# Kernel optimization log

Hardware: AMD Instinct MI355X
Metric: run time of the kernel (lower is better)

The kernel has to match this reference:

```python
import jax, jax.numpy as jnp
import numpy as np


def setup_inputs() -> dict:
    key = jax.random.key(0)
    k1, k2, k3 = jax.random.split(key, 3)
    B, C, H, W = 64, 512, 28, 28
    K = 32
    std = 1.0 / (K * C) ** 0.5
    x = jax.random.normal(k1, (B, C, H, W), dtype=jnp.float32)
    codewords = jax.random.uniform(k2, (K, C), dtype=jnp.float32, minval=-std, maxval=std)
    scale = jax.random.uniform(k3, (K,), dtype=jnp.float32, minval=-1.0, maxval=0.0)
    return {"x": x, "codewords": codewords, "scale": scale}


def reference(x, codewords, scale):
    # x: (B, C, H, W) -> descriptors (B, N, C)
    B, C, H, W = x.shape
    K = codewords.shape[0]
    xd = x.reshape(B, C, H * W).transpose(0, 2, 1)  # (B, N, C)

    # scaled L2: scale_k * ||x_n - c_k||^2, expanded without (B,N,K,C) intermediate
    x_sq = jnp.sum(xd * xd, axis=-1, keepdims=True)            # (B, N, 1)
    c_sq = jnp.sum(codewords * codewords, axis=-1)             # (K,)
    xc = jnp.einsum("bnc,kc->bnk", xd, codewords)              # (B, N, K)
    dist = scale * (x_sq - 2.0 * xc + c_sq)                    # (B, N, K)

    A = jax.nn.softmax(dist, axis=2)                           # (B, N, K)

    # encoded_k = sum_n A[b,n,k] * (x[b,n] - c[k])
    wx = jnp.einsum("bnk,bnc->bkc", A, xd)                     # (B, K, C)
    wsum = jnp.sum(A, axis=1)                                  # (B, K)
    encoded = wx - wsum[:, :, None] * codewords[None, :, :]    # (B, K, C)
    return encoded
```

## Files before the change

kernel.cpp:

```cpp
#include <hip/hip_runtime.h>
#include <hip/hip_bf16.h>

#define BB 64
#define CC 512
#define NPIX 784
#define KK 32
#define NSPL 7
#define PXB 112
#define CW_S 520
#define XA_S 136

typedef __attribute__((ext_vector_type(8))) short short8;
typedef __attribute__((ext_vector_type(4))) float floatx4;
typedef __attribute__((ext_vector_type(4))) unsigned short ushort4v;

#define OFF_WP 0
#define OFF_WS (NSPL*BB*KK*CC)

__device__ __forceinline__ unsigned short f2bf(float f) {
    union { float f; unsigned u; } v; v.f = f;
    return (unsigned short)((v.u + 0x7FFFu + ((v.u >> 16) & 1u)) >> 16);
}
__device__ __forceinline__ float bf2f(unsigned short h) {
    union { unsigned u; float f; } v; v.u = ((unsigned)h) << 16; return v.f;
}

__global__ __launch_bounds__(256) void k_fused(const float* __restrict__ x,
                                               const float* __restrict__ cw,
                                               const float* __restrict__ scale,
                                               float* __restrict__ ws)
{
    __shared__ __align__(16) unsigned char u8[128 * XA_S * 2];
    __shared__ __align__(16) unsigned short A_l[KK * XA_S];
    __shared__ float csq_p[8][KK];
    __shared__ float csq_l[KK];
    __shared__ float wred[KK][8];

    unsigned short* cs = (unsigned short*)u8;
    unsigned short* xs = (unsigned short*)u8;

    const int t     = threadIdx.x;
    const int lane  = t & 63;
    const int w     = t >> 6;
    const int col   = lane & 15;
    const int quad  = lane >> 4;
    const int split = blockIdx.x;
    const int b     = blockIdx.y;
    const int p0    = split * PXB;

#pragma unroll 4
    for (int j = 0; j < 16; ++j) {
        const int qidx = t + j * 256;
        const int row = qidx >> 7, qc = qidx & 127;
        const float4 v = *(const float4*)&cw[row * CC + qc * 4];
        ushort4v p; p.x = f2bf(v.x); p.y = f2bf(v.y); p.z = f2bf(v.z); p.w = f2bf(v.w);
        *(ushort4v*)&cs[row * CW_S + qc * 4] = p;
    }
    __syncthreads();
    {
        const int k = t & 31, part = t >> 5;
        float s = 0.f;
        for (int i = 0; i < 64; ++i) {
            const float v = bf2f(cs[k * CW_S + part * 64 + i]);
            s += v * v;
        }
        csq_p[part][k] = s;
    }
    __syncthreads();
    if (t < KK) {
        float s = 0.f;
#pragma unroll
        for (int p = 0; p < 8; ++p) s += csq_p[p][t];
        csq_l[t] = s;
    }
    __syncthreads();

    const float s0 = scale[col], s1 = scale[col + 16];
    const float q0 = csq_l[col], q1 = csq_l[col + 16];

    for (int pt = w; pt < NSPL; pt += 4) {
        const int px = p0 + pt * 16 + col;
        const float* xb = x + (size_t)b * CC * NPIX + px;

        floatx4 acc0 = {0.f, 0.f, 0.f, 0.f};
        floatx4 acc1 = {0.f, 0.f, 0.f, 0.f};
        float xsqp = 0.f;
        float va[8], vb[8];

#pragma unroll
        for (int j = 0; j < 8; ++j) va[j] = xb[(size_t)(quad * 8 + j) * NPIX];

#pragma unroll
        for (int kc = 0; kc < 16; kc += 2) {
            {
                const int cb = (kc + 1) * 32 + quad * 8;
#pragma unroll
                for (int j = 0; j < 8; ++j) vb[j] = xb[(size_t)(cb + j) * NPIX];
            }
            {
#pragma unroll
                for (int j = 0; j < 8; ++j) xsqp += va[j] * va[j];
                short8 a;
#pragma unroll
                for (int j = 0; j < 8; ++j) a[j] = (short)f2bf(va[j]);
                const int cb0 = kc * 32 + quad * 8;
                const short8 b0 = *(const short8*)&cs[col * CW_S + cb0];
                const short8 b1 = *(const short8*)&cs[(col + 16) * CW_S + cb0];
                acc0 = __builtin_amdgcn_mfma_f32_16x16x32_bf16(a, b0, acc0, 0, 0, 0);
                acc1 = __builtin_amdgcn_mfma_f32_16x16x32_bf16(a, b1, acc1, 0, 0, 0);
            }
            if (kc + 2 < 16) {
                const int cb = (kc + 2) * 32 + quad * 8;
#pragma unroll
                for (int j = 0; j < 8; ++j) va[j] = xb[(size_t)(cb + j) * NPIX];
            }
            {
#pragma unroll
                for (int j = 0; j < 8; ++j) xsqp += vb[j] * vb[j];
                short8 a;
#pragma unroll
                for (int j = 0; j < 8; ++j) a[j] = (short)f2bf(vb[j]);
                const int cb1 = (kc + 1) * 32 + quad * 8;
                const short8 b0 = *(const short8*)&cs[col * CW_S + cb1];
                const short8 b1 = *(const short8*)&cs[(col + 16) * CW_S + cb1];
                acc0 = __builtin_amdgcn_mfma_f32_16x16x32_bf16(a, b0, acc0, 0, 0, 0);
                acc1 = __builtin_amdgcn_mfma_f32_16x16x32_bf16(a, b1, acc1, 0, 0, 0);
            }
        }

        xsqp += __shfl_xor(xsqp, 16);
        xsqp += __shfl_xor(xsqp, 32);

#pragma unroll
        for (int r = 0; r < 4; ++r) {
            const float xq = __shfl(xsqp, quad * 4 + r);
            const float d0 = s0 * (xq + q0 - 2.f * acc0[r]);
            const float d1 = s1 * (xq + q1 - 2.f * acc1[r]);
            float mx = fmaxf(d0, d1);
            mx = fmaxf(mx, __shfl_xor(mx, 1));
            mx = fmaxf(mx, __shfl_xor(mx, 2));
            mx = fmaxf(mx, __shfl_xor(mx, 4));
            mx = fmaxf(mx, __shfl_xor(mx, 8));
            const float e0 = __expf(d0 - mx), e1 = __expf(d1 - mx);
            float sm = e0 + e1;
            sm += __shfl_xor(sm, 1);
            sm += __shfl_xor(sm, 2);
            sm += __shfl_xor(sm, 4);
            sm += __shfl_xor(sm, 8);
            const float inv = 1.f / sm;
            const int pxl = pt * 16 + quad * 4 + r;
            A_l[col * XA_S + pxl]        = f2bf(e0 * inv);
            A_l[(col + 16) * XA_S + pxl] = f2bf(e1 * inv);
        }
    }
    __syncthreads();

    {
        const int k = t >> 3, part = t & 7;
        float s = 0.f;
#pragma unroll 7
        for (int i = 0; i < 14; ++i) s += bf2f(A_l[k * XA_S + part * 14 + i]);
        wred[k][part] = s;
    }
    {
        const ushort4v z = {0, 0, 0, 0};
        if (t < 128) *(ushort4v*)&A_l[(t >> 2) * XA_S + PXB + (t & 3) * 4] = z;
#pragma unroll
        for (int jj = 0; jj < 2; ++jj) {
            const int q = t + jj * 256;
            *(ushort4v*)&xs[(q >> 2) * XA_S + PXB + (q & 3) * 4] = z;
        }
    }
    __syncthreads();

    if (t < KK) {
        float s = 0.f;
#pragma unroll
        for (int p = 0; p < 8; ++p) s += wred[t][p];
        ws[OFF_WS + (size_t)(split * BB + b) * KK + t] = s;
    }

    const float* xbase = x + (size_t)b * CC * NPIX + p0;
    float* Wp = ws + OFF_WP;

    for (int cch = 0; cch < 4; ++cch) {
#pragma unroll 2
        for (int j = 0; j < 14; ++j) {
            const int q = t + j * 256;
            const int row = q / 28, pq = q - row * 28;
            const float4 v = *(const float4*)&xbase[(size_t)(cch * 128 + row) * NPIX + pq * 4];
            ushort4v p; p.x = f2bf(v.x); p.y = f2bf(v.y); p.z = f2bf(v.z); p.w = f2bf(v.w);
            *(ushort4v*)&xs[row * XA_S + pq * 4] = p;
        }
        __syncthreads();

        floatx4 a00 = {0.f,0.f,0.f,0.f}, a01 = {0.f,0.f,0.f,0.f};
        floatx4 a10 = {0.f,0.f,0.f,0.f}, a11 = {0.f,0.f,0.f,0.f};
#pragma unroll
        for (int ks = 0; ks < 4; ++ks) {
            const int off = ks * 32 + quad * 8;
            const short8 av0 = *(const short8*)&A_l[col * XA_S + off];
            const short8 av1 = *(const short8*)&A_l[(col + 16) * XA_S + off];
            const short8 bv0 = *(const short8*)&xs[(w * 32 + col) * XA_S + off];
            const short8 bv1 = *(const short8*)&xs[(w * 32 + 16 + col) * XA_S + off];
            a00 = __builtin_amdgcn_mfma_f32_16x16x32_bf16(av0, bv0, a00, 0, 0, 0);
            a10 = __builtin_amdgcn_mfma_f32_16x16x32_bf16(av1, bv0, a10, 0, 0, 0);
            a01 = __builtin_amdgcn_mfma_f32_16x16x32_bf16(av0, bv1, a01, 0, 0, 0);
            a11 = __builtin_amdgcn_mfma_f32_16x16x32_bf16(av1, bv1, a11, 0, 0, 0);
        }

        const size_t sb = (size_t)(split * BB + b) * KK;
        const int cb = cch * 128 + w * 32;
#pragma unroll
        for (int r = 0; r < 4; ++r) {
            const int k0 = quad * 4 + r;
            Wp[(sb + k0) * CC + cb + col]           = a00[r];
            Wp[(sb + k0) * CC + cb + 16 + col]      = a01[r];
            Wp[(sb + k0 + 16) * CC + cb + col]      = a10[r];
            Wp[(sb + k0 + 16) * CC + cb + 16 + col] = a11[r];
        }
        __syncthreads();
    }
}

__global__ __launch_bounds__(256) void k3(const float* __restrict__ cw,
                                          const float* __restrict__ ws,
                                          float* __restrict__ out)
{
    const int idx = blockIdx.x * 256 + threadIdx.x;
    const int c4 = idx & 127;
    const int k  = (idx >> 7) & 31;
    const int b  = idx >> 12;

    const float* Wp = ws + OFF_WP;
    float4 s = make_float4(0.f, 0.f, 0.f, 0.f);
#pragma unroll
    for (int sp = 0; sp < NSPL; ++sp) {
        const float4 v = *(const float4*)&Wp[((size_t)(sp * BB + b) * KK + k) * CC + c4 * 4];
        s.x += v.x; s.y += v.y; s.z += v.z; s.w += v.w;
    }
    float wsum = 0.f;
#pragma unroll
    for (int sp = 0; sp < NSPL; ++sp) wsum += ws[OFF_WS + (size_t)(sp * BB + b) * KK + k];

    const float4 c4f = *(const float4*)&cw[k * CC + c4 * 4];
    float4 o;
    o.x = s.x - wsum * c4f.x;
    o.y = s.y - wsum * c4f.y;
    o.z = s.z - wsum * c4f.z;
    o.w = s.w - wsum * c4f.w;
    *(float4*)&out[(size_t)idx * 4] = o;
}

extern "C" void kernel_launch(void* const* d_in, const int* in_sizes, int n_in,
                              void* d_out, int out_size, void* d_ws, size_t ws_size,
                              hipStream_t stream) {
    const float* x     = (const float*)d_in[0];
    const float* cw    = (const float*)d_in[1];
    const float* scale = (const float*)d_in[2];
    float* out = (float*)d_out;
    float* ws  = (float*)d_ws;

    k_fused<<<dim3(NSPL, BB), dim3(256), 0, stream>>>(x, cw, scale, ws);
    k3<<<dim3(BB * KK * CC / 4 / 256), dim3(256), 0, stream>>>(cw, ws, out);
}
```

Baseline: 185.4 us.

## Split pixels into 13 blocks of 64 with one pixel tile per wave

Each block now covers 64 pixels instead of 112, giving 13 splits per batch instead of 7. Each of the four waves handles exactly one 16-pixel tile, and the tail past 784 pixels is handled by clamped loads and zero-masked writes. This replaces the separate padding pass and moves a barrier. The aim is more blocks for better GPU occupancy and less per-block serial work. In exchange it writes more partial results to the workspace (13 splits instead of 7), which the reduction kernel must read back. The codebook bf16 conversion and norm work is also repeated in more blocks.

```diff
diff --git a/kernel.cpp b/kernel.cpp
--- a/kernel.cpp
+++ b/kernel.cpp
@@ -5,10 +5,10 @@
 #define CC 512
 #define NPIX 784
 #define KK 32
-#define NSPL 7
-#define PXB 112
+#define NSPL 13
+#define PXB 64
 #define CW_S 520
-#define XA_S 136
+#define XS2_S 72
 
 typedef __attribute__((ext_vector_type(8))) short short8;
 typedef __attribute__((ext_vector_type(4))) float floatx4;
@@ -30,8 +30,8 @@
                                                const float* __restrict__ scale,
                                                float* __restrict__ ws)
 {
-    __shared__ __align__(16) unsigned char u8[128 * XA_S * 2];
-    __shared__ __align__(16) unsigned short A_l[KK * XA_S];
+    __shared__ __align__(16) unsigned char u8[KK * CW_S * 2];
+    __shared__ __align__(16) unsigned short A_l[KK * XS2_S];
     __shared__ float csq_p[8][KK];
     __shared__ float csq_l[KK];
     __shared__ float wred[KK][8];
@@ -78,8 +78,9 @@
     const float s0 = scale[col], s1 = scale[col + 16];
     const float q0 = csq_l[col], q1 = csq_l[col + 16];
 
-    for (int pt = w; pt < NSPL; pt += 4) {
-        const int px = p0 + pt * 16 + col;
+    {
+        const int pxg = p0 + w * 16 + col;
+        const int px = (pxg < NPIX) ? pxg : (NPIX - 1);
         const float* xb = x + (size_t)b * CC * NPIX + px;
 
         floatx4 acc0 = {0.f, 0.f, 0.f, 0.f};
@@ -133,6 +134,7 @@
 
 #pragma unroll
         for (int r = 0; r < 4; ++r) {
+            const int pl = w * 16 + quad * 4 + r;
             const float xq = __shfl(xsqp, quad * 4 + r);
             const float d0 = s0 * (xq + q0 - 2.f * acc0[r]);
             const float d1 = s1 * (xq + q1 - 2.f * acc1[r]);
@@ -148,9 +150,9 @@
             sm += __shfl_xor(sm, 4);
             sm += __shfl_xor(sm, 8);
             const float inv = 1.f / sm;
-            const int pxl = pt * 16 + quad * 4 + r;
-            A_l[col * XA_S + pxl]        = f2bf(e0 * inv);
-            A_l[(col + 16) * XA_S + pxl] = f2bf(e1 * inv);
+            const bool valid = (p0 + pl) < NPIX;
+            A_l[col * XS2_S + pl]        = valid ? f2bf(e0 * inv) : (unsigned short)0;
+            A_l[(col + 16) * XS2_S + pl] = valid ? f2bf(e1 * inv) : (unsigned short)0;
         }
     }
     __syncthreads();
@@ -158,21 +160,11 @@
     {
         const int k = t >> 3, part = t & 7;
         float s = 0.f;
-#pragma unroll 7
-        for (int i = 0; i < 14; ++i) s += bf2f(A_l[k * XA_S + part * 14 + i]);
+#pragma unroll
+        for (int i = 0; i < 8; ++i) s += bf2f(A_l[k * XS2_S + part * 8 + i]);
         wred[k][part] = s;
     }
-    {
-        const ushort4v z = {0, 0, 0, 0};
-        if (t < 128) *(ushort4v*)&A_l[(t >> 2) * XA_S + PXB + (t & 3) * 4] = z;
-#pragma unroll
-        for (int jj = 0; jj < 2; ++jj) {
-            const int q = t + jj * 256;
-            *(ushort4v*)&xs[(q >> 2) * XA_S + PXB + (q & 3) * 4] = z;
-        }
-    }
-    __syncthreads();
-
+    __syncthreads();
     if (t < KK) {
         float s = 0.f;
 #pragma unroll
@@ -184,25 +176,29 @@
     float* Wp = ws + OFF_WP;
 
     for (int cch = 0; cch < 4; ++cch) {
+        __syncthreads();
 #pragma unroll 2
-        for (int j = 0; j < 14; ++j) {
+        for (int j = 0; j < 8; ++j) {
             const int q = t + j * 256;
-            const int row = q / 28, pq = q - row * 28;
-            const float4 v = *(const float4*)&xbase[(size_t)(cch * 128 + row) * NPIX + pq * 4];
-            ushort4v p; p.x = f2bf(v.x); p.y = f2bf(v.y); p.z = f2bf(v.z); p.w = f2bf(v.w);
-            *(ushort4v*)&xs[row * XA_S + pq * 4] = p;
+            const int row = q >> 4, pq = q & 15;
+            ushort4v p;
+            if (p0 + pq * 4 < NPIX) {
+                const float4 v = *(const float4*)&xbase[(size_t)(cch * 128 + row) * NPIX + pq * 4];
+                p.x = f2bf(v.x); p.y = f2bf(v.y); p.z = f2bf(v.z); p.w = f2bf(v.w);
+            } else { p.x = 0; p.y = 0; p.z = 0; p.w = 0; }
+            *(ushort4v*)&xs[row * XS2_S + pq * 4] = p;
         }
         __syncthreads();
 
         floatx4 a00 = {0.f,0.f,0.f,0.f}, a01 = {0.f,0.f,0.f,0.f};
         floatx4 a10 = {0.f,0.f,0.f,0.f}, a11 = {0.f,0.f,0.f,0.f};
 #pragma unroll
-        for (int ks = 0; ks < 4; ++ks) {
+        for (int ks = 0; ks < 2; ++ks) {
             const int off = ks * 32 + quad * 8;
-            const short8 av0 = *(const short8*)&A_l[col * XA_S + off];
-            const short8 av1 = *(const short8*)&A_l[(col + 16) * XA_S + off];
-            const short8 bv0 = *(const short8*)&xs[(w * 32 + col) * XA_S + off];
-            const short8 bv1 = *(const short8*)&xs[(w * 32 + 16 + col) * XA_S + off];
+            const short8 av0 = *(const short8*)&A_l[col * XS2_S + off];
+            const short8 av1 = *(const short8*)&A_l[(col + 16) * XS2_S + off];
+            const short8 bv0 = *(const short8*)&xs[(w * 32 + col) * XS2_S + off];
+            const short8 bv1 = *(const short8*)&xs[(w * 32 + 16 + col) * XS2_S + off];
             a00 = __builtin_amdgcn_mfma_f32_16x16x32_bf16(av0, bv0, a00, 0, 0, 0);
             a10 = __builtin_amdgcn_mfma_f32_16x16x32_bf16(av1, bv0, a10, 0, 0, 0);
             a01 = __builtin_amdgcn_mfma_f32_16x16x32_bf16(av0, bv1, a01, 0, 0, 0);
@@ -219,7 +215,6 @@
             Wp[(sb + k0 + 16) * CC + cb + col]      = a10[r];
             Wp[(sb + k0 + 16) * CC + cb + 16 + col] = a11[r];
         }
-        __syncthreads();
     }
 }
 
```

Result: slower. 192.3 us (+3.7%).
